# Performance work log

Measured on AMD Instinct MI355X. Metric: run time of the kernel, lower is better.

Reference implementation:

```python
import jax, jax.numpy as jnp
import numpy as np

SEQ_LEN = 4096
D_IN = 2048
D_OUT = 2048
DROPOUT_P = 0.5


def setup_inputs() -> dict:
    key = jax.random.key(0)
    kx, kq, kk, kv = jax.random.split(key, 4)
    return {
        "x": jax.random.normal(kx, (SEQ_LEN, D_IN), dtype=jnp.float32),
        "W_query": jax.random.uniform(kq, (D_IN, D_OUT), dtype=jnp.float32),
        "W_key": jax.random.uniform(kk, (D_IN, D_OUT), dtype=jnp.float32),
        "W_value": jax.random.uniform(kv, (D_IN, D_OUT), dtype=jnp.float32),
    }


def reference(x, W_query, W_key, W_value):
    # projections: [S, d_in] @ [d_in, d_out] -> [S, d_out]
    queries = x @ W_query
    keys = x @ W_key
    values = x @ W_value
    # full score matrix [S, S]
    attn_scores = queries @ keys.T
    S = attn_scores.shape[0]
    causal_mask = jnp.triu(jnp.ones((S, S), dtype=bool), k=1)
    masked = jnp.where(causal_mask, -jnp.inf, attn_scores)
    scale = jnp.sqrt(jnp.asarray(keys.shape[-1], dtype=masked.dtype))
    attn_weights = jax.nn.softmax(masked / scale, axis=1)
    # dropout p=0.5 (train mode), inverted scaling, deterministic key
    keep = jax.random.bernoulli(jax.random.key(42), 1.0 - DROPOUT_P, attn_weights.shape)
    attn_weights = jnp.where(keep, attn_weights / (1.0 - DROPOUT_P), 0.0)
    context_vec = attn_weights @ values  # [S, d_out]
    return context_vec
```

## Files before the change

### kernel.cpp

```cpp
#include <hip/hip_runtime.h>
#include <cstdint>
#include <cstddef>
#include <cmath>

#define SEQ 4096
#define DM  2048
#define NSC ((SEQ / 128) * (SEQ / 128 + 1) / 2)

typedef unsigned int u32;
typedef unsigned short u16;
typedef __attribute__((ext_vector_type(8))) short bf16x8;
typedef __attribute__((ext_vector_type(4))) float f32x4;

__device__ __forceinline__ u16 f2bf(float f) {
  u32 u = __float_as_uint(f);
  return (u16)((u + 0x7FFFu + ((u >> 16) & 1u)) >> 16);
}
__device__ __forceinline__ float bf2f(u16 h) { return __uint_as_float(((u32)h) << 16); }

__device__ __forceinline__ u32 rotl32(u32 x, int r) { return (x << r) | (x >> (32 - r)); }

__device__ __forceinline__ void tf2x32(u32 c0, u32 c1, u32& o0, u32& o1) {
  const u32 k0 = 0u, k1 = 42u, k2 = 0x1BD11BDAu ^ 0u ^ 42u;
  u32 x0 = c0 + k0;
  u32 x1 = c1 + k1;
#define TFR(r) { x0 += x1; x1 = rotl32(x1, (r)); x1 ^= x0; }
  TFR(13) TFR(15) TFR(26) TFR(6)   x0 += k1; x1 += k2 + 1u;
  TFR(17) TFR(29) TFR(16) TFR(24)  x0 += k2; x1 += k0 + 2u;
  TFR(13) TFR(15) TFR(26) TFR(6)   x0 += k0; x1 += k1 + 3u;
  TFR(17) TFR(29) TFR(16) TFR(24)  x0 += k1; x1 += k2 + 4u;
  TFR(13) TFR(15) TFR(26) TFR(6)   x0 += k2; x1 += k0 + 5u;
#undef TFR
  o0 = x0; o1 = x1;
}

__device__ __forceinline__ bool dropout_keep(u32 idx) {
  u32 a, b; tf2x32(0u, idx, a, b);
  return (((a ^ b) & 0x80000000u) == 0u);
}

__device__ __forceinline__ void g2l16(const void* g, void* l) {
  __builtin_amdgcn_global_load_lds((const __attribute__((address_space(1))) u32*)g,
                                   (__attribute__((address_space(3))) u32*)l, 16, 0, 0);
}

#define MFMA16(a, b, c) __builtin_amdgcn_mfma_f32_16x16x32_bf16(a, b, c, 0, 0, 0)


__device__ __forceinline__ void gemm_core_split(
    const u16* __restrict__ Ah, const u16* __restrict__ AlFT,
    const u16* __restrict__ Bh, const u16* __restrict__ BlFT,
    int lda, int ldb, int rowBlock, int colBlock, int kmax,
    f32x4 (&acc)[4][4], u16* smem)
{
  u16* Als = smem;
  u16* Bls = smem + 8192;
  const int tid  = threadIdx.x;
  const int wid  = tid >> 6;
  const int lane = tid & 63;
  const int wr   = (wid & 1) << 6;
  const int wc   = (wid >> 1) << 6;
  const int lrow = lane & 15;
  const int lk   = (((lane >> 4) ^ ((lrow >> 1) & 3)) << 3);
  const int srow = wid * 32 + (lane >> 2);
  const int skol = (((lane & 3) ^ ((lane >> 3) & 3)) << 3);
  const int KA32 = lda >> 5, KB32 = ldb >> 5;
  const int rtA = (rowBlock >> 4) + ((wid & 1) << 2);
  const int rtB = (colBlock >> 4) + ((wid >> 1) << 2);

  const f32x4 zero = {0.f, 0.f, 0.f, 0.f};
#pragma unroll
  for (int i = 0; i < 4; ++i)
#pragma unroll
    for (int j = 0; j < 4; ++j) acc[i][j] = zero;

  for (int kb = 0; kb < kmax; kb += 64) {
#pragma unroll
    for (int h = 0; h < 2; ++h)
#pragma unroll
      for (int t = 0; t < 2; ++t) {
        const size_t ga = (size_t)(rowBlock + srow + t * 16) * lda + kb + h * 32 + skol;
        const size_t gb = (size_t)(colBlock + srow + t * 16) * ldb + kb + h * 32 + skol;
        const int lo = h * 4096 + (wid * 32 + t * 16) * 32;
        g2l16(Ah + ga, &Als[lo]);
        g2l16(Bh + gb, &Bls[lo]);
      }
    __syncthreads();

#pragma unroll
    for (int h = 0; h < 2; ++h) {
      const int kt = (kb >> 5) + h;
      bf16x8 al[4], bl[4], ah[4], bh[4];
#pragma unroll
      for (int r = 0; r < 4; ++r) {
        al[r] = *(const bf16x8*)(AlFT + (((size_t)(rtA + r) * KA32 + kt) * 64 + lane) * 8);
        bl[r] = *(const bf16x8*)(BlFT + (((size_t)(rtB + r) * KB32 + kt) * 64 + lane) * 8);
        ah[r] = *(const bf16x8*)&Als[h * 4096 + (wr + r * 16 + lrow) * 32 + lk];
        bh[r] = *(const bf16x8*)&Bls[h * 4096 + (wc + r * 16 + lrow) * 32 + lk];
      }
#pragma unroll
      for (int r = 0; r < 4; ++r)
#pragma unroll
        for (int c = 0; c < 4; ++c) {
          acc[r][c] = MFMA16(ah[r], bh[c], acc[r][c]);
          acc[r][c] = MFMA16(ah[r], bl[c], acc[r][c]);
          acc[r][c] = MFMA16(al[r], bh[c], acc[r][c]);
        }
    }
    __syncthreads();
  }
}

__device__ __forceinline__ void gemm_core(
    const u16* __restrict__ Ah, const u16* __restrict__ Bh,
    int lda, int ldb, int rowBlock, int colBlock, int kmax,
    f32x4 (&acc)[4][4], u16* smem)
{
  u16* Als = smem;
  u16* Bls = smem + 8192;
  const int tid  = threadIdx.x;
  const int wid  = tid >> 6;
  const int lane = tid & 63;
  const int wr   = (wid & 1) << 6;
  const int wc   = (wid >> 1) << 6;
  const int lrow = lane & 15;
  const int lk   = (((lane >> 4) ^ ((lrow >> 1) & 3)) << 3);
  const int srow = wid * 32 + (lane >> 2);
  const int skol = (((lane & 3) ^ ((lane >> 3) & 3)) << 3);

  const f32x4 zero = {0.f, 0.f, 0.f, 0.f};
#pragma unroll
  for (int i = 0; i < 4; ++i)
#pragma unroll
    for (int j = 0; j < 4; ++j) acc[i][j] = zero;

  for (int kb = 0; kb < kmax; kb += 64) {
#pragma unroll
    for (int h = 0; h < 2; ++h)
#pragma unroll
      for (int t = 0; t < 2; ++t) {
        const size_t ga = (size_t)(rowBlock + srow + t * 16) * lda + kb + h * 32 + skol;
        const size_t gb = (size_t)(colBlock + srow + t * 16) * ldb + kb + h * 32 + skol;
        const int lo = h * 4096 + (wid * 32 + t * 16) * 32;
        g2l16(Ah + ga, &Als[lo]);
        g2l16(Bh + gb, &Bls[lo]);
      }
    __syncthreads();

#pragma unroll
    for (int h = 0; h < 2; ++h) {
      bf16x8 ah[4], bh[4];
#pragma unroll
      for (int r = 0; r < 4; ++r) {
        ah[r] = *(const bf16x8*)&Als[h * 4096 + (wr + r * 16 + lrow) * 32 + lk];
        bh[r] = *(const bf16x8*)&Bls[h * 4096 + (wc + r * 16 + lrow) * 32 + lk];
      }
#pragma unroll
      for (int r = 0; r < 4; ++r)
#pragma unroll
        for (int c = 0; c < 4; ++c)
          acc[r][c] = MFMA16(ah[r], bh[c], acc[r][c]);
    }
    __syncthreads();
  }
}

__global__ __launch_bounds__(256) void k_split_all(
    const float* __restrict__ X, u16* __restrict__ Xh, u16* __restrict__ Xl,
    const float* __restrict__ Wq, const float* __restrict__ Wk, const float* __restrict__ Wv,
    u16* __restrict__ Wqh, u16* __restrict__ Wql,
    u16* __restrict__ Wkh, u16* __restrict__ Wkl, u16* __restrict__ Wvh) {
  __shared__ float t[64][65];
  const int bid = blockIdx.x;
  const int tid = threadIdx.x;
  const int wid = tid >> 6, lane = tid & 63;

  if (bid < 4096) {
    const int kt = bid & 63;
    const int rt = (bid >> 6) * 4 + wid;
    const int row = rt * 16 + (lane & 15);
    const int col = kt * 32 + ((lane >> 4) << 3);
    const float* src = X + (size_t)row * DM + col;
    const float4 v0 = *(const float4*)src;
    const float4 v1 = *(const float4*)(src + 4);
    float v[8] = {v0.x, v0.y, v0.z, v0.w, v1.x, v1.y, v1.z, v1.w};
    u16 h[8], l[8];
#pragma unroll
    for (int j = 0; j < 8; ++j) {
      h[j] = f2bf(v[j]);
      l[j] = f2bf(v[j] - bf2f(h[j]));
    }
    u16* hp = Xh + (size_t)row * DM + col;
    *(ushort4*)hp = *(ushort4*)&h[0];
    *(ushort4*)(hp + 4) = *(ushort4*)&h[4];
    u16* lp = Xl + (((size_t)rt * 64 + kt) * 64 + lane) * 8;
    *(ushort4*)lp = *(ushort4*)&l[0];
    *(ushort4*)(lp + 4) = *(ushort4*)&l[4];
    return;
  }

  const int r = bid - 4096;
  const int z = r >> 10;
  const int rem = r & 1023;
  const int n0 = (rem & 31) * 64, k0 = (rem >> 5) * 64;
  const float* W = (z == 0) ? Wq : (z == 1) ? Wk : Wv;
  u16* Oh = (z == 0) ? Wqh : (z == 1) ? Wkh : Wvh;
  u16* Ol = (z == 0) ? Wql : Wkl;
  const int tx = tid & 63, ty = tid >> 6;
#pragma unroll
  for (int i = 0; i < 16; ++i)
    t[ty * 16 + i][tx] = W[(size_t)(k0 + ty * 16 + i) * DM + n0 + tx];
  __syncthreads();
  {
    const int nl = tid >> 2, kc = (tid & 3) * 16;
    u16 h[16];
#pragma unroll
    for (int i = 0; i < 16; ++i) h[i] = f2bf(t[kc + i][nl]);
    u16* hp = Oh + (size_t)(n0 + nl) * DM + k0 + kc;
#pragma unroll
    for (int i = 0; i < 4; ++i) *(ushort4*)(hp + i * 4) = *(ushort4*)&h[i * 4];
  }
  if (z < 2) {
#pragma unroll
    for (int kt = 0; kt < 2; ++kt) {
      const int nl = wid * 16 + (lane & 15);
      const int kc = kt * 32 + ((lane >> 4) << 3);
      u16 l[8];
#pragma unroll
      for (int j = 0; j < 8; ++j) {
        const float v = t[kc + j][nl];
        l[j] = f2bf(v - bf2f(f2bf(v)));
      }
      const int rtg = (n0 >> 4) + wid, ktg = (k0 >> 5) + kt;
      u16* lp = Ol + (((size_t)rtg * 64 + ktg) * 64 + lane) * 8;
      *(ushort4*)lp = *(ushort4*)&l[0];
      *(ushort4*)(lp + 4) = *(ushort4*)&l[4];
    }
  }
}

__global__ __launch_bounds__(256) void k_proj_qkv(
    const u16* __restrict__ Xh, const u16* __restrict__ Xl,
    const u16* __restrict__ Wqh, const u16* __restrict__ Wql,
    const u16* __restrict__ Wkh, const u16* __restrict__ Wkl,
    const u16* __restrict__ Wvh,
    u16* __restrict__ Qh, u16* __restrict__ Ql,
    u16* __restrict__ Kh, u16* __restrict__ Kl,
    u16* __restrict__ Vt, float rscaleQ)
{
  __shared__ __align__(16) u16 smem[16384];
  const int z = blockIdx.z;
  const int rowBlock = blockIdx.y * 128, colBlock = blockIdx.x * 128;
  const int lane = threadIdx.x & 63, wid = threadIdx.x >> 6;

  if (z == 2) {
    f32x4 acc[4][4];
    gemm_core(Xh, Wvh, DM, DM, rowBlock, colBlock, DM, acc, smem);
    const int r0 = rowBlock + ((wid & 1) << 6) + ((lane >> 4) << 2);
    const int c0 = colBlock + ((wid >> 1) << 6) + (lane & 15);
#pragma unroll
    for (int r = 0; r < 4; ++r)
#pragma unroll
      for (int c = 0; c < 4; ++c) {
        ushort4 pk;
        pk.x = f2bf(acc[r][c][0]); pk.y = f2bf(acc[r][c][1]);
        pk.z = f2bf(acc[r][c][2]); pk.w = f2bf(acc[r][c][3]);
        *(ushort4*)(Vt + (size_t)(c0 + c * 16) * SEQ + r0 + r * 16) = pk;
      }
    return;
  }

  const u16* Bh = z ? Wkh : Wqh;
  const u16* Bl = z ? Wkl : Wql;
  u16* Oh = z ? Kh : Qh;
  u16* Ol = z ? Kl : Ql;
  const float rs = z ? 1.0f : rscaleQ;
  f32x4 acc[4][4];
  gemm_core_split(Xh, Xl, Bh, Bl, DM, DM, rowBlock, colBlock, DM, acc, smem);

  const int lr0 = ((wid & 1) << 6) + ((lane >> 4) << 2);
  const int lc0 = ((wid >> 1) << 6) + (lane & 15);
#pragma unroll
  for (int r = 0; r < 4; ++r)
#pragma unroll
    for (int c = 0; c < 4; ++c)
#pragma unroll
      for (int e = 0; e < 4; ++e) {
        const float v = acc[r][c][e] * rs;
        const u16 h = f2bf(v);
        const int lrow = lr0 + r * 16 + e, lcol = lc0 + c * 16;
        Oh[(size_t)(rowBlock + lrow) * DM + colBlock + lcol] = h;
        smem[lrow * 128 + lcol] = f2bf(v - bf2f(h));
      }
  __syncthreads();
#pragma unroll
  for (int t8 = 0; t8 < 8; ++t8) {
    const int idx = wid * 8 + t8;
    const int rt = idx >> 2, kt = idx & 3;
    u16 l[8];
#pragma unroll
    for (int j = 0; j < 8; ++j)
      l[j] = smem[(rt * 16 + (lane & 15)) * 128 + kt * 32 + ((lane >> 4) << 3) + j];
    const int rtg = (rowBlock >> 4) + rt, ktg = (colBlock >> 5) + kt;
    u16* lp = Ol + (((size_t)rtg * (DM / 32) + ktg) * 64 + lane) * 8;
    *(ushort4*)lp = *(ushort4*)&l[0];
    *(ushort4*)(lp + 4) = *(ushort4*)&l[4];
  }
}

__global__ __launch_bounds__(256) void k_scores(
    const u16* __restrict__ Qh, const u16* __restrict__ Ql,
    const u16* __restrict__ Kh, const u16* __restrict__ Kl, float* __restrict__ S)
{
  __shared__ __align__(16) u16 smem[16384];
  const int bid = blockIdx.x;
  int by = (int)((sqrtf(8.0f * (float)bid + 1.0f) - 1.0f) * 0.5f);
  while ((by + 1) * (by + 2) / 2 <= bid) ++by;
  while (by * (by + 1) / 2 > bid) --by;
  const int bx = bid - by * (by + 1) / 2;

  f32x4 acc[4][4];
  gemm_core_split(Qh, Ql, Kh, Kl, DM, DM, by * 128, bx * 128, DM, acc, smem);

  const int lane = threadIdx.x & 63, wid = threadIdx.x >> 6;
  const int r0 = by * 128 + ((wid & 1) << 6) + ((lane >> 4) << 2);
  const int c0 = bx * 128 + ((wid >> 1) << 6) + (lane & 15);
#pragma unroll
  for (int r = 0; r < 4; ++r)
#pragma unroll
    for (int c = 0; c < 4; ++c)
#pragma unroll
      for (int e = 0; e < 4; ++e)
        S[(size_t)(r0 + r * 16 + e) * SEQ + (c0 + c * 16)] = acc[r][c][e];
}

__global__ __launch_bounds__(256) void k_softmax_dropout(const float* __restrict__ S,
                                                         u16* __restrict__ P) {
  const int row = blockIdx.x;
  const int n = row + 1;
  const int nt = (n + 1023) >> 10;
  const int tid = threadIdx.x;
  __shared__ float buf[SEQ];
  __shared__ float red[4];
  __shared__ float bcast;
  const float* srow = S + (size_t)row * SEQ;

  float lmax = -INFINITY;
  for (int t = 0; t < nt; ++t) {
    int j4 = tid + t * 256;
    float4 v = *(const float4*)(srow + (size_t)j4 * 4);
    int b = j4 * 4;
    float x0 = (b + 0 < n) ? v.x : -INFINITY;
    float x1 = (b + 1 < n) ? v.y : -INFINITY;
    float x2 = (b + 2 < n) ? v.z : -INFINITY;
    float x3 = (b + 3 < n) ? v.w : -INFINITY;
    buf[b + 0] = x0; buf[b + 1] = x1; buf[b + 2] = x2; buf[b + 3] = x3;
    lmax = fmaxf(lmax, fmaxf(fmaxf(x0, x1), fmaxf(x2, x3)));
  }
  for (int off = 32; off > 0; off >>= 1) lmax = fmaxf(lmax, __shfl_down(lmax, off, 64));
  if ((tid & 63) == 0) red[tid >> 6] = lmax;
  __syncthreads();
  if (tid == 0) bcast = fmaxf(fmaxf(red[0], red[1]), fmaxf(red[2], red[3]));
  __syncthreads();
  const float m = bcast;

  float lsum = 0.f;
  for (int t = 0; t < nt; ++t) {
    int b = (tid + t * 256) * 4;
    float e0 = expf(buf[b + 0] - m);
    float e1 = expf(buf[b + 1] - m);
    float e2 = expf(buf[b + 2] - m);
    float e3 = expf(buf[b + 3] - m);
    buf[b + 0] = e0; buf[b + 1] = e1; buf[b + 2] = e2; buf[b + 3] = e3;
    lsum += (e0 + e1) + (e2 + e3);
  }
  for (int off = 32; off > 0; off >>= 1) lsum += __shfl_down(lsum, off, 64);
  if ((tid & 63) == 0) red[tid >> 6] = lsum;
  __syncthreads();
  if (tid == 0) bcast = (red[0] + red[1]) + (red[2] + red[3]);
  __syncthreads();
  const float total = bcast;

  u16* prow = P + (size_t)row * SEQ;
  const int zeroEnd = ((row >> 7) + 1) << 7;
  for (int j = tid; j < zeroEnd; j += 256) {
    float out = 0.f;
    if (j < n) {
      const float w = buf[j] / total;
      out = dropout_keep((u32)(row * SEQ + j)) ? w * 2.0f : 0.f;
    }
    prow[j] = f2bf(out);
  }
}

__global__ __launch_bounds__(256) void k_pv(const u16* __restrict__ P,
                                            const u16* __restrict__ Vt,
                                            float* __restrict__ O) {
  __shared__ __align__(16) u16 smem[16384];
  const int by = (SEQ / 128 - 1) - blockIdx.y;
  f32x4 acc[4][4];
  gemm_core(P, Vt, SEQ, SEQ, by * 128, blockIdx.x * 128, (by + 1) * 128, acc, smem);

  const int lane = threadIdx.x & 63, wid = threadIdx.x >> 6;
  const int r0 = by * 128 + ((wid & 1) << 6) + ((lane >> 4) << 2);
  const int c0 = blockIdx.x * 128 + ((wid >> 1) << 6) + (lane & 15);
#pragma unroll
  for (int r = 0; r < 4; ++r)
#pragma unroll
    for (int c = 0; c < 4; ++c)
#pragma unroll
      for (int e = 0; e < 4; ++e)
        O[(size_t)(r0 + r * 16 + e) * DM + (c0 + c * 16)] = acc[r][c][e];
}

extern "C" void kernel_launch(void* const* d_in, const int* in_sizes, int n_in,
                              void* d_out, int out_size, void* d_ws, size_t ws_size,
                              hipStream_t stream) {
  const float* x  = (const float*)d_in[0];
  const float* Wq = (const float*)d_in[1];
  const float* Wk = (const float*)d_in[2];
  const float* Wv = (const float*)d_in[3];

  const size_t PL = (size_t)SEQ * DM;
  const size_t WL = (size_t)DM * DM;
  u16* base = (u16*)d_ws;
  u16* Qh = base;
  u16* Ql = Qh + PL;
  u16* Kh = Ql + PL;
  u16* Kl = Kh + PL;
  u16* Vt = Kl + PL;
  u16* P  = base;
  u16* regA = Vt + PL;
  u16* Xh  = regA;
  u16* Xl  = Xh + PL;
  u16* Wqh = Xl + PL;
  u16* Wql = Wqh + WL;
  u16* Wkh = Wql + WL;
  u16* Wkl = Wkh + WL;
  u16* Wvh = Wkl + WL;
  float* S = (float*)regA;

  const float rscale = 1.0f / sqrtf(2048.0f);
  dim3 blk(256);
  k_split_all<<<dim3(4096 + 3 * 1024), blk, 0, stream>>>(x, Xh, Xl, Wq, Wk, Wv,
                                                         Wqh, Wql, Wkh, Wkl, Wvh);
  k_proj_qkv<<<dim3(DM / 128, SEQ / 128, 3), blk, 0, stream>>>(
      Xh, Xl, Wqh, Wql, Wkh, Wkl, Wvh, Qh, Ql, Kh, Kl, Vt, rscale);
  k_scores<<<dim3(NSC), blk, 0, stream>>>(Qh, Ql, Kh, Kl, S);
  k_softmax_dropout<<<dim3(SEQ), blk, 0, stream>>>(S, P);
  k_pv<<<dim3(DM / 128, SEQ / 128), blk, 0, stream>>>(P, Vt, (float*)d_out);
}
```

Before: 665.2 us.

## Switch split-bf16 GEMM core to 32x32x16 MFMA with matching low-part layout

Replaces the 16x16x32 bf16 MFMA tiles in the split-precision GEMM core with 32x32x16 MFMA tiles, using 2x2 accumulators of 16 floats per wave. The pre-tiled low-part layouts written by the split and projection kernels are changed to 32-row by 16-k fragments to match, and the LDS staging of Q/K low parts now uses an XOR swizzle with vector reads. The aim is fewer MFMA issues and fewer fragment loads per unit of work, since the larger instruction gives more reuse per operand load. The trade-off is more loop iterations per k-block, different register pressure, and changed global store patterns in the epilogues.

```diff
diff --git a/kernel.cpp b/kernel.cpp
--- a/kernel.cpp
+++ b/kernel.cpp
@@ -11,6 +11,7 @@
 typedef unsigned short u16;
 typedef __attribute__((ext_vector_type(8))) short bf16x8;
 typedef __attribute__((ext_vector_type(4))) float f32x4;
+typedef __attribute__((ext_vector_type(16))) float f32x16;
 
 __device__ __forceinline__ u16 f2bf(float f) {
   u32 u = __float_as_uint(f);
@@ -45,13 +46,14 @@
 }
 
 #define MFMA16(a, b, c) __builtin_amdgcn_mfma_f32_16x16x32_bf16(a, b, c, 0, 0, 0)
+#define MFMA32(a, b, c) __builtin_amdgcn_mfma_f32_32x32x16_bf16(a, b, c, 0, 0, 0)
 
 
 __device__ __forceinline__ void gemm_core_split(
     const u16* __restrict__ Ah, const u16* __restrict__ AlFT,
     const u16* __restrict__ Bh, const u16* __restrict__ BlFT,
     int lda, int ldb, int rowBlock, int colBlock, int kmax,
-    f32x4 (&acc)[4][4], u16* smem)
+    f32x16 (&acc)[2][2], u16* smem)
 {
   u16* Als = smem;
   u16* Bls = smem + 8192;
@@ -60,19 +62,20 @@
   const int lane = tid & 63;
   const int wr   = (wid & 1) << 6;
   const int wc   = (wid >> 1) << 6;
-  const int lrow = lane & 15;
-  const int lk   = (((lane >> 4) ^ ((lrow >> 1) & 3)) << 3);
+  const int l31  = lane & 31;
+  const int lh   = lane >> 5;
   const int srow = wid * 32 + (lane >> 2);
   const int skol = (((lane & 3) ^ ((lane >> 3) & 3)) << 3);
-  const int KA32 = lda >> 5, KB32 = ldb >> 5;
-  const int rtA = (rowBlock >> 4) + ((wid & 1) << 2);
-  const int rtB = (colBlock >> 4) + ((wid >> 1) << 2);
-
-  const f32x4 zero = {0.f, 0.f, 0.f, 0.f};
-#pragma unroll
-  for (int i = 0; i < 4; ++i)
-#pragma unroll
-    for (int j = 0; j < 4; ++j) acc[i][j] = zero;
+  const int KA16 = lda >> 4, KB16 = ldb >> 4;
+  const int rtA0 = (rowBlock >> 5) + ((wid & 1) << 1);
+  const int rtB0 = (colBlock >> 5) + ((wid >> 1) << 1);
+  const int swz  = (l31 >> 1) & 3;
+
+  const f32x16 zero = {0.f,0.f,0.f,0.f,0.f,0.f,0.f,0.f,0.f,0.f,0.f,0.f,0.f,0.f,0.f,0.f};
+#pragma unroll
+  for (int i = 0; i < 2; ++i)
+#pragma unroll
+    for (int j = 0; j < 2; ++j) acc[i][j] = zero;
 
   for (int kb = 0; kb < kmax; kb += 64) {
 #pragma unroll
@@ -88,23 +91,27 @@
     __syncthreads();
 
 #pragma unroll
-    for (int h = 0; h < 2; ++h) {
-      const int kt = (kb >> 5) + h;
-      bf16x8 al[4], bl[4], ah[4], bh[4];
-#pragma unroll
-      for (int r = 0; r < 4; ++r) {
-        al[r] = *(const bf16x8*)(AlFT + (((size_t)(rtA + r) * KA32 + kt) * 64 + lane) * 8);
-        bl[r] = *(const bf16x8*)(BlFT + (((size_t)(rtB + r) * KB32 + kt) * 64 + lane) * 8);
-        ah[r] = *(const bf16x8*)&Als[h * 4096 + (wr + r * 16 + lrow) * 32 + lk];
-        bh[r] = *(const bf16x8*)&Bls[h * 4096 + (wc + r * 16 + lrow) * 32 + lk];
-      }
-#pragma unroll
-      for (int r = 0; r < 4; ++r)
-#pragma unroll
-        for (int c = 0; c < 4; ++c) {
-          acc[r][c] = MFMA16(ah[r], bh[c], acc[r][c]);
-          acc[r][c] = MFMA16(ah[r], bl[c], acc[r][c]);
-          acc[r][c] = MFMA16(al[r], bh[c], acc[r][c]);
+    for (int q = 0; q < 4; ++q) {
+      const int h = q >> 1, s = q & 1;
+      const int kt16 = (kb >> 4) + q;
+      const int cl = s * 2 + lh;
+      bf16x8 ah[2], bh[2], al[2], bl[2];
+#pragma unroll
+      for (int r = 0; r < 2; ++r) {
+        const int rowA = wr + r * 32 + l31;
+        const int rowB = wc + r * 32 + l31;
+        ah[r] = *(const bf16x8*)&Als[h * 4096 + rowA * 32 + ((cl ^ swz) << 3)];
+        bh[r] = *(const bf16x8*)&Bls[h * 4096 + rowB * 32 + ((cl ^ swz) << 3)];
+        al[r] = *(const bf16x8*)(AlFT + (((size_t)(rtA0 + r) * KA16 + kt16) * 64 + lane) * 8);
+        bl[r] = *(const bf16x8*)(BlFT + (((size_t)(rtB0 + r) * KB16 + kt16) * 64 + lane) * 8);
+      }
+#pragma unroll
+      for (int r = 0; r < 2; ++r)
+#pragma unroll
+        for (int c = 0; c < 2; ++c) {
+          acc[r][c] = MFMA32(ah[r], bh[c], acc[r][c]);
+          acc[r][c] = MFMA32(ah[r], bl[c], acc[r][c]);
+          acc[r][c] = MFMA32(al[r], bh[c], acc[r][c]);
         }
     }
     __syncthreads();
@@ -176,10 +183,10 @@
   const int wid = tid >> 6, lane = tid & 63;
 
   if (bid < 4096) {
-    const int kt = bid & 63;
-    const int rt = (bid >> 6) * 4 + wid;
-    const int row = rt * 16 + (lane & 15);
-    const int col = kt * 32 + ((lane >> 4) << 3);
+    const int kt16 = bid & 127;
+    const int rt32 = (bid >> 7) * 4 + wid;
+    const int row = rt32 * 32 + (lane & 31);
+    const int col = kt16 * 16 + ((lane >> 5) << 3);
     const float* src = X + (size_t)row * DM + col;
     const float4 v0 = *(const float4*)src;
     const float4 v1 = *(const float4*)(src + 4);
@@ -193,7 +200,7 @@
     u16* hp = Xh + (size_t)row * DM + col;
     *(ushort4*)hp = *(ushort4*)&h[0];
     *(ushort4*)(hp + 4) = *(ushort4*)&h[4];
-    u16* lp = Xl + (((size_t)rt * 64 + kt) * 64 + lane) * 8;
+    u16* lp = Xl + (((size_t)rt32 * 128 + kt16) * 64 + lane) * 8;
     *(ushort4*)lp = *(ushort4*)&l[0];
     *(ushort4*)(lp + 4) = *(ushort4*)&l[4];
     return;
@@ -222,17 +229,19 @@
   }
   if (z < 2) {
 #pragma unroll
-    for (int kt = 0; kt < 2; ++kt) {
-      const int nl = wid * 16 + (lane & 15);
-      const int kc = kt * 32 + ((lane >> 4) << 3);
+    for (int tt = 0; tt < 2; ++tt) {
+      const int idx = wid * 2 + tt;
+      const int rt = idx >> 2, kt = idx & 3;
+      const int nl = rt * 32 + (lane & 31);
+      const int kc = kt * 16 + ((lane >> 5) << 3);
       u16 l[8];
 #pragma unroll
       for (int j = 0; j < 8; ++j) {
         const float v = t[kc + j][nl];
         l[j] = f2bf(v - bf2f(f2bf(v)));
       }
-      const int rtg = (n0 >> 4) + wid, ktg = (k0 >> 5) + kt;
-      u16* lp = Ol + (((size_t)rtg * 64 + ktg) * 64 + lane) * 8;
+      const int rtg = (n0 >> 5) + rt, ktg = (k0 >> 4) + kt;
+      u16* lp = Ol + (((size_t)rtg * (DM / 16) + ktg) * 64 + lane) * 8;
       *(ushort4*)lp = *(ushort4*)&l[0];
       *(ushort4*)(lp + 4) = *(ushort4*)&l[4];
     }
@@ -275,36 +284,39 @@
   u16* Oh = z ? Kh : Qh;
   u16* Ol = z ? Kl : Ql;
   const float rs = z ? 1.0f : rscaleQ;
-  f32x4 acc[4][4];
+  f32x16 acc[2][2];
   gemm_core_split(Xh, Xl, Bh, Bl, DM, DM, rowBlock, colBlock, DM, acc, smem);
 
-  const int lr0 = ((wid & 1) << 6) + ((lane >> 4) << 2);
-  const int lc0 = ((wid >> 1) << 6) + (lane & 15);
-#pragma unroll
-  for (int r = 0; r < 4; ++r)
-#pragma unroll
-    for (int c = 0; c < 4; ++c)
-#pragma unroll
-      for (int e = 0; e < 4; ++e) {
-        const float v = acc[r][c][e] * rs;
-        const u16 h = f2bf(v);
-        const int lrow = lr0 + r * 16 + e, lcol = lc0 + c * 16;
-        Oh[(size_t)(rowBlock + lrow) * DM + colBlock + lcol] = h;
-        smem[lrow * 128 + lcol] = f2bf(v - bf2f(h));
-      }
+  const int wr = (wid & 1) << 6, wc = (wid >> 1) << 6;
+  const int l31 = lane & 31, lh = lane >> 5;
+#pragma unroll
+  for (int r = 0; r < 2; ++r)
+#pragma unroll
+    for (int c = 0; c < 2; ++c) {
+      const int colL = wc + c * 32 + l31;
+      const int colG = colBlock + colL;
+#pragma unroll
+      for (int g = 0; g < 4; ++g)
+#pragma unroll
+        for (int e = 0; e < 4; ++e) {
+          const int rowL = wr + r * 32 + 4 * lh + e + 8 * g;
+          const float v = acc[r][c][g * 4 + e] * rs;
+          const u16 h = f2bf(v);
+          Oh[(size_t)(rowBlock + rowL) * DM + colG] = h;
+          smem[rowL * 128 + (((colL >> 3) ^ (rowL & 7)) << 3) + (colL & 7)] =
+              f2bf(v - bf2f(h));
+        }
+    }
   __syncthreads();
 #pragma unroll
   for (int t8 = 0; t8 < 8; ++t8) {
     const int idx = wid * 8 + t8;
-    const int rt = idx >> 2, kt = idx & 3;
-    u16 l[8];
-#pragma unroll
-    for (int j = 0; j < 8; ++j)
-      l[j] = smem[(rt * 16 + (lane & 15)) * 128 + kt * 32 + ((lane >> 4) << 3) + j];
-    const int rtg = (rowBlock >> 4) + rt, ktg = (colBlock >> 5) + kt;
-    u16* lp = Ol + (((size_t)rtg * (DM / 32) + ktg) * 64 + lane) * 8;
-    *(ushort4*)lp = *(ushort4*)&l[0];
-    *(ushort4*)(lp + 4) = *(ushort4*)&l[4];
+    const int rt = idx >> 3, kt = idx & 7;
+    const int rowL = rt * 32 + l31;
+    const int ch = kt * 2 + lh;
+    const bf16x8 vL = *(const bf16x8*)&smem[rowL * 128 + ((ch ^ (rowL & 7)) << 3)];
+    const int rtg = (rowBlock >> 5) + rt, ktg = (colBlock >> 4) + kt;
+    *(bf16x8*)(Ol + (((size_t)rtg * (DM / 16) + ktg) * 64 + lane) * 8) = vL;
   }
 }
 
@@ -319,19 +331,26 @@
   while (by * (by + 1) / 2 > bid) --by;
   const int bx = bid - by * (by + 1) / 2;
 
-  f32x4 acc[4][4];
+  f32x16 acc[2][2];
   gemm_core_split(Qh, Ql, Kh, Kl, DM, DM, by * 128, bx * 128, DM, acc, smem);
 
   const int lane = threadIdx.x & 63, wid = threadIdx.x >> 6;
-  const int r0 = by * 128 + ((wid & 1) << 6) + ((lane >> 4) << 2);
-  const int c0 = bx * 128 + ((wid >> 1) << 6) + (lane & 15);
-#pragma unroll
-  for (int r = 0; r < 4; ++r)
-#pragma unroll
-    for (int c = 0; c < 4; ++c)
-#pragma unroll
-      for (int e = 0; e < 4; ++e)
-        S[(size_t)(r0 + r * 16 + e) * SEQ + (c0 + c * 16)] = acc[r][c][e];
+  const int wr = (wid & 1) << 6, wc = (wid >> 1) << 6;
+  const int l31 = lane & 31, lh = lane >> 5;
+  const int r0 = by * 128 + wr, c0 = bx * 128 + wc;
+#pragma unroll
+  for (int r = 0; r < 2; ++r)
+#pragma unroll
+    for (int c = 0; c < 2; ++c) {
+      const int col = c0 + c * 32 + l31;
+#pragma unroll
+      for (int g = 0; g < 4; ++g)
+#pragma unroll
+        for (int e = 0; e < 4; ++e) {
+          const int row = r0 + r * 32 + 4 * lh + e + 8 * g;
+          S[(size_t)row * SEQ + col] = acc[r][c][g * 4 + e];
+        }
+    }
 }
 
 __global__ __launch_bounds__(256) void k_softmax_dropout(const float* __restrict__ S,
```

Measured after the change: 656.9 us. About the same (-1.2%).
